# Performance work log

Hardware: AMD Instinct MI355X
Metric: run time of the kernel (lower is better)

## Reference

```python
import jax, jax.numpy as jnp
import numpy as np

KH, KW = 3, 3
STRIDE, PAD, DIL = 1, 1, 1
GROUPS, DG = 1, 1
B, C, H, W = 4, 64, 96, 96
O = 64
K = KH * KW


def setup_inputs() -> dict:
    key = jax.random.key(0)
    k1, k2, k3, k4 = jax.random.split(key, 4)
    x = jax.random.normal(k1, (B, C, H, W), dtype=jnp.float32)
    offset = jax.random.normal(k2, (B, DG * 2 * K, H, W), dtype=jnp.float32)
    mask = jax.random.uniform(k3, (B, DG * K, H, W), dtype=jnp.float32)
    stdv = 1.0 / np.sqrt(C * KH * KW)
    weight = jax.random.uniform(k4, (O, C // GROUPS, KH, KW), dtype=jnp.float32,
                                minval=-stdv, maxval=stdv)
    bias = jnp.zeros((O,), dtype=jnp.float32)
    return {"x": x, "offset": offset, "mask": mask, "weight": weight, "bias": bias}


def _dcn(x, offset, mask, weight, bias):
    Bc, Cc, Hc, Wc = x.shape
    Ho = (Hc + 2 * PAD - DIL * (KH - 1) - 1) // STRIDE + 1
    Wo = (Wc + 2 * PAD - DIL * (KW - 1) - 1) // STRIDE + 1
    Cg = Cc // DG
    dt = x.dtype

    # offset channels per deform group: [k, (y,x)] interleaved (mmcv layout)
    off = offset.reshape(Bc, DG, K, 2, Ho, Wo)
    off_y, off_x = off[:, :, :, 0], off[:, :, :, 1]          # [B,DG,K,Ho,Wo]
    m = mask.reshape(Bc, DG, K, Ho, Wo)

    ky = (jnp.arange(K) // KW).astype(dt) * DIL               # kernel tap dy
    kx = (jnp.arange(K) % KW).astype(dt) * DIL                # kernel tap dx
    base_y = (jnp.arange(Ho) * STRIDE - PAD).astype(dt)
    base_x = (jnp.arange(Wo) * STRIDE - PAD).astype(dt)
    py = base_y[None, None, None, :, None] + ky[None, None, :, None, None] + off_y
    px = base_x[None, None, None, None, :] + kx[None, None, :, None, None] + off_x

    y0 = jnp.floor(py)
    x0 = jnp.floor(px)
    ly = py - y0
    lx = px - x0
    y0i = y0.astype(jnp.int32)
    x0i = x0.astype(jnp.int32)

    x_flat = x.reshape(Bc, DG, Cg, Hc * Wc)

    def gather(yi, xi):
        # zero-padding semantics: out-of-range corners contribute 0
        valid = ((yi >= 0) & (yi < Hc) & (xi >= 0) & (xi < Wc)).astype(dt)
        idx = jnp.clip(yi, 0, Hc - 1) * Wc + jnp.clip(xi, 0, Wc - 1)
        idx_b = jnp.broadcast_to(idx.reshape(Bc, DG, 1, K * Ho * Wo),
                                 (Bc, DG, Cg, K * Ho * Wo))
        vals = jnp.take_along_axis(x_flat, idx_b, axis=3)
        return vals.reshape(Bc, DG, Cg, K, Ho, Wo), valid

    v00, m00 = gather(y0i, x0i)
    v01, m01 = gather(y0i, x0i + 1)
    v10, m10 = gather(y0i + 1, x0i)
    v11, m11 = gather(y0i + 1, x0i + 1)

    w00 = ((1 - ly) * (1 - lx) * m00)[:, :, None]             # [B,DG,1,K,Ho,Wo]
    w01 = ((1 - ly) * lx * m01)[:, :, None]
    w10 = (ly * (1 - lx) * m10)[:, :, None]
    w11 = (ly * lx * m11)[:, :, None]

    sampled = v00 * w00 + v01 * w01 + v10 * w10 + v11 * w11   # bilinear
    sampled = sampled * m[:, :, None]                         # mask modulation
    s = sampled.reshape(Bc, Cc, K, Ho, Wo)

    out = jnp.einsum('ock,bckhw->bohw', weight.reshape(O, Cc, K), s)
    return out + bias[None, :, None, None]


def reference(x, offset, mask, weight, bias):
    return _dcn(x, offset, mask, weight, bias)
```

## Files before the change

kernel.cpp:

```cpp
#include <hip/hip_runtime.h>

#define Bn 4
#define Cn 64
#define Hn 96
#define Wn 96
#define On 64
#define Kn 9
#define HWn (Hn*Wn)
#define NT 256
#define TP 16
#define TW (Wn/TP)
#define TG 3
#define NGRP (TW/TG)
#define NBLK (Bn*Hn*NGRP)
#define WR 9
#define WC 24
#define XSTR 72
#define NPIX (WR*WC)
#define SSTRIDE 584
#define NKT 18

typedef __attribute__((ext_vector_type(8))) short bf16x8;
typedef __attribute__((ext_vector_type(4))) short bf16x4;
typedef __attribute__((ext_vector_type(4))) float f32x4;
typedef __attribute__((ext_vector_type(4))) unsigned u32x4;

__device__ __forceinline__ unsigned short f2bf(float f) {
    unsigned u = __float_as_uint(f);
    u += 0x7FFFu + ((u >> 16) & 1u);
    return (unsigned short)(u >> 16);
}
__device__ __forceinline__ float bf2f(unsigned short h) {
    return __uint_as_float((unsigned)h << 16);
}
__device__ __forceinline__ unsigned cvtpk(float a, float b) {
    return (unsigned)f2bf(a) | ((unsigned)f2bf(b) << 16);
}

__global__ __launch_bounds__(NT, 3) void dcn_fused_kernel(
    const float* __restrict__ x, const float* __restrict__ offset,
    const float* __restrict__ mask, const float* __restrict__ w,
    const float* __restrict__ bias, float* __restrict__ out)
{
    __shared__ __align__(16) unsigned short xwin[NPIX * XSTR];
    __shared__ __align__(16) unsigned short Slds[TP * SSTRIDE];
    __shared__ float4 lwv[4][36];
    __shared__ int    lbs[4][36];

    const int tid  = threadIdx.x;
    const int wave = tid >> 6;
    const int lane = tid & 63;

    const int p = blockIdx.x;
    const int v = (p & 7) * (NBLK / 8) + (p >> 3);
    const int b   = v / (Hn * NGRP);
    int rem       = v - b * (Hn * NGRP);
    const int ho  = rem / NGRP;
    const int grp = rem - ho * NGRP;
    const int wr0 = ho - 4;

    bf16x8 afrag[NKT];
    {
        const float* wrow = w + ((wave * 16 + (lane & 15)) * (Cn * Kn))
                              + ((lane >> 4) * 8);
        #pragma unroll
        for (int t = 0; t < NKT; ++t) {
            float4 fa = *(const float4*)(wrow + t * 32);
            float4 fb = *(const float4*)(wrow + t * 32 + 4);
            u32x4 u;
            u.x = cvtpk(fa.x, fa.y);
            u.y = cvtpk(fa.z, fa.w);
            u.z = cvtpk(fb.x, fb.y);
            u.w = cvtpk(fb.z, fb.w);
            afrag[t] = __builtin_bit_cast(bf16x8, u);
        }
    }

    for (int s = 0; s < TG; ++s) {
        const int wt  = grp * TG + s;
        const int wo0 = wt * TP;
        const int wc0 = wo0 - 4;

        {
            const float* xb = x + (size_t)b * Cn * HWn;
            #pragma unroll 4
            for (int i = 0; i < (Cn / 2 * NPIX) / NT; ++i) {
                int e   = i * NT + tid;
                int cp  = e / NPIX;
                int pix = e - cp * NPIX;
                int r   = pix / WC;
                int col = pix - r * WC;
                int gr = wr0 + r, gc = wc0 + col;
                bool ok = (gr >= 0) && (gr < Hn) && (gc >= 0) && (gc < Wn);
                int cgr = min(max(gr, 0), Hn - 1);
                int cgc = min(max(gc, 0), Wn - 1);
                const float* src = xb + (size_t)(2 * cp) * HWn + cgr * Wn + cgc;
                float v0 = src[0];
                float v1 = src[HWn];
                if (!ok) { v0 = 0.f; v1 = 0.f; }
                *(unsigned*)&xwin[pix * XSTR + 2 * cp] = cvtpk(v0, v1);
            }
        }

        if (lane < 36) {
            const int k  = lane >> 2;
            const int pl = lane & 3;
            const int wo = wo0 + wave * 4 + pl;
            float oy = offset[((b * (2*Kn) + 2*k    ) * Hn + ho) * Wn + wo];
            float ox = offset[((b * (2*Kn) + 2*k + 1) * Hn + ho) * Wn + wo];
            float mm = mask  [((b * Kn + k) * Hn + ho) * Wn + wo];
            float py = (float)(ho - 1 + (k / 3)) + oy;
            float px = (float)(wo - 1 + (k % 3)) + ox;
            float y0f = floorf(py), x0f = floorf(px);
            float ly = py - y0f, lx = px - x0f;
            int y0 = (int)y0f, x0i = (int)x0f;
            float vy0 = (y0     >= 0 && y0     < Hn) ? 1.f : 0.f;
            float vy1 = (y0 + 1 >= 0 && y0 + 1 < Hn) ? 1.f : 0.f;
            float vx0 = (x0i    >= 0 && x0i    < Wn) ? 1.f : 0.f;
            float vx1 = (x0i+ 1 >= 0 && x0i+ 1 < Wn) ? 1.f : 0.f;
            float4 wv;
            wv.x = (1.f - ly) * (1.f - lx) * mm * vy0 * vx0;
            wv.y = (1.f - ly) * lx         * mm * vy0 * vx1;
            wv.z = ly         * (1.f - lx) * mm * vy1 * vx0;
            wv.w = ly         * lx         * mm * vy1 * vx1;
            lwv[wave][lane] = wv;
            int ry = y0 - wr0, rx = x0i - wc0;
            bool fast = (ry >= 0) && (ry <= WR - 2) && (rx >= 0) && (rx <= WC - 2);
            lbs[wave][lane] = fast ? (ry * WC + rx) : -1;
        }
        __syncthreads();

        {
            const int pl  = lane >> 4;
            const int q   = lane & 15;
            const int gpx = wave * 4 + pl;
            unsigned short* Srow = &Slds[gpx * SSTRIDE];
            #pragma unroll
            for (int k = 0; k < Kn; ++k) {
                float4 wv = lwv[wave][k * 4 + pl];
                int base  = lbs[wave][k * 4 + pl];
                float f[4];
                if (base >= 0) {
                    const unsigned short* ppix = &xwin[base * XSTR + q * 4];
                    bf16x4 v0 = *(const bf16x4*)(ppix);
                    bf16x4 v1 = *(const bf16x4*)(ppix + XSTR);
                    bf16x4 v2 = *(const bf16x4*)(ppix + WC * XSTR);
                    bf16x4 v3 = *(const bf16x4*)(ppix + WC * XSTR + XSTR);
                    #pragma unroll
                    for (int j = 0; j < 4; ++j) {
                        f[j] = wv.x * bf2f((unsigned short)v0[j])
                             + wv.y * bf2f((unsigned short)v1[j])
                             + wv.z * bf2f((unsigned short)v2[j])
                             + wv.w * bf2f((unsigned short)v3[j]);
                    }
                } else {
                    const int wo = wo0 + gpx;
                    float oy = offset[((b * (2*Kn) + 2*k    ) * Hn + ho) * Wn + wo];
                    float ox = offset[((b * (2*Kn) + 2*k + 1) * Hn + ho) * Wn + wo];
                    float py = (float)(ho - 1 + (k / 3)) + oy;
                    float px = (float)(wo - 1 + (k % 3)) + ox;
                    int y0 = (int)floorf(py), x0i = (int)floorf(px);
                    int cy0 = min(max(y0,     0), Hn - 1);
                    int cy1 = min(max(y0 + 1, 0), Hn - 1);
                    int cx0 = min(max(x0i,     0), Wn - 1);
                    int cx1 = min(max(x0i + 1, 0), Wn - 1);
                    int i00 = cy0 * Wn + cx0, i01 = cy0 * Wn + cx1;
                    int i10 = cy1 * Wn + cx0, i11 = cy1 * Wn + cx1;
                    const float* xc = x + ((size_t)b * Cn + q * 4) * HWn;
                    #pragma unroll
                    for (int j = 0; j < 4; ++j) {
                        const float* xj = xc + (size_t)j * HWn;
                        f[j] = wv.x * xj[i00] + wv.y * xj[i01]
                             + wv.z * xj[i10] + wv.w * xj[i11];
                    }
                }
                unsigned p01 = cvtpk(f[0], f[1]);
                unsigned p23 = cvtpk(f[2], f[3]);
                Srow[(q * 4 + 0) * Kn + k] = (unsigned short)(p01);
                Srow[(q * 4 + 1) * Kn + k] = (unsigned short)(p01 >> 16);
                Srow[(q * 4 + 2) * Kn + k] = (unsigned short)(p23);
                Srow[(q * 4 + 3) * Kn + k] = (unsigned short)(p23 >> 16);
            }
        }
        __syncthreads();

        {
            const int n    = lane & 15;
            const int quad = lane >> 4;
            f32x4 acc = {0.f, 0.f, 0.f, 0.f};
            #pragma unroll
            for (int t = 0; t < NKT; ++t) {
                bf16x8 bFrag = *(const bf16x8*)&Slds[n * SSTRIDE + t * 32 + quad * 8];
                acc = __builtin_amdgcn_mfma_f32_16x16x32_bf16(afrag[t], bFrag, acc, 0, 0, 0);
            }
            #pragma unroll
            for (int r = 0; r < 4; ++r) {
                int o = wave * 16 + quad * 4 + r;
                out[(((size_t)b * On + o) * Hn + ho) * Wn + wo0 + n] = acc[r] + bias[o];
            }
        }
    }
}

extern "C" void kernel_launch(void* const* d_in, const int* in_sizes, int n_in,
                              void* d_out, int out_size, void* d_ws, size_t ws_size,
                              hipStream_t stream) {
    (void)in_sizes; (void)n_in; (void)out_size; (void)d_ws; (void)ws_size;
    dcn_fused_kernel<<<NBLK, NT, 0, stream>>>(
        (const float*)d_in[0], (const float*)d_in[1], (const float*)d_in[2],
        (const float*)d_in[3], (const float*)d_in[4], (float*)d_out);
}
```

Baseline: 109.5 us.

## Reorder GEMM reduction to tap-major, vectorize S stores, restructure window load

Result: no change. 107.7 us (-1.6%).

```diff
diff --git a/kernel.cpp b/kernel.cpp
--- a/kernel.cpp
+++ b/kernel.cpp
@@ -15,7 +15,7 @@
 #define NBLK (Bn*Hn*NGRP)
 #define WR 9
 #define WC 24
-#define XSTR 72
+#define XSTR 68
 #define NPIX (WR*WC)
 #define SSTRIDE 584
 #define NKT 18
@@ -61,17 +61,20 @@
 
     bf16x8 afrag[NKT];
     {
-        const float* wrow = w + ((wave * 16 + (lane & 15)) * (Cn * Kn))
-                              + ((lane >> 4) * 8);
+        const int o  = wave * 16 + (lane & 15);
+        const int hi = lane >> 4;
+        const float* wlane = w + (size_t)o * (Cn * Kn) + hi * 8 * Kn;
         #pragma unroll
         for (int t = 0; t < NKT; ++t) {
-            float4 fa = *(const float4*)(wrow + t * 32);
-            float4 fb = *(const float4*)(wrow + t * 32 + 4);
+            const float* src = wlane + (t & 1) * 32 * Kn + (t >> 1);
+            float f[8];
+            #pragma unroll
+            for (int j = 0; j < 8; ++j) f[j] = src[j * Kn];
             u32x4 u;
-            u.x = cvtpk(fa.x, fa.y);
-            u.y = cvtpk(fa.z, fa.w);
-            u.z = cvtpk(fb.x, fb.y);
-            u.w = cvtpk(fb.z, fb.w);
+            u.x = cvtpk(f[0], f[1]);
+            u.y = cvtpk(f[2], f[3]);
+            u.z = cvtpk(f[4], f[5]);
+            u.w = cvtpk(f[6], f[7]);
             afrag[t] = __builtin_bit_cast(bf16x8, u);
         }
     }
@@ -81,24 +84,23 @@
         const int wo0 = wt * TP;
         const int wc0 = wo0 - 4;
 
-        {
-            const float* xb = x + (size_t)b * Cn * HWn;
-            #pragma unroll 4
-            for (int i = 0; i < (Cn / 2 * NPIX) / NT; ++i) {
-                int e   = i * NT + tid;
-                int cp  = e / NPIX;
-                int pix = e - cp * NPIX;
-                int r   = pix / WC;
-                int col = pix - r * WC;
-                int gr = wr0 + r, gc = wc0 + col;
-                bool ok = (gr >= 0) && (gr < Hn) && (gc >= 0) && (gc < Wn);
-                int cgr = min(max(gr, 0), Hn - 1);
-                int cgc = min(max(gc, 0), Wn - 1);
-                const float* src = xb + (size_t)(2 * cp) * HWn + cgr * Wn + cgc;
-                float v0 = src[0];
-                float v1 = src[HWn];
-                if (!ok) { v0 = 0.f; v1 = 0.f; }
-                *(unsigned*)&xwin[pix * XSTR + 2 * cp] = cvtpk(v0, v1);
+        if (tid < NPIX) {
+            const int r   = tid / WC;
+            const int col = tid - r * WC;
+            const int gr = wr0 + r, gc = wc0 + col;
+            unsigned short* dst = &xwin[tid * XSTR];
+            if ((gr >= 0) & (gr < Hn) & (gc >= 0) & (gc < Wn)) {
+                const float* src = x + (size_t)b * Cn * HWn + gr * Wn + gc;
+                #pragma unroll 8
+                for (int cp = 0; cp < Cn / 2; ++cp) {
+                    float v0 = src[(2 * cp) * HWn];
+                    float v1 = src[(2 * cp + 1) * HWn];
+                    *(unsigned*)&dst[2 * cp] = cvtpk(v0, v1);
+                }
+            } else {
+                #pragma unroll 8
+                for (int cp = 0; cp < Cn / 2; ++cp)
+                    *(unsigned*)&dst[2 * cp] = 0u;
             }
         }
 
@@ -174,12 +176,10 @@
                              + wv.z * xj[i10] + wv.w * xj[i11];
                     }
                 }
-                unsigned p01 = cvtpk(f[0], f[1]);
-                unsigned p23 = cvtpk(f[2], f[3]);
-                Srow[(q * 4 + 0) * Kn + k] = (unsigned short)(p01);
-                Srow[(q * 4 + 1) * Kn + k] = (unsigned short)(p01 >> 16);
-                Srow[(q * 4 + 2) * Kn + k] = (unsigned short)(p23);
-                Srow[(q * 4 + 3) * Kn + k] = (unsigned short)(p23 >> 16);
+                uint2 pk;
+                pk.x = cvtpk(f[0], f[1]);
+                pk.y = cvtpk(f[2], f[3]);
+                *(uint2*)&Slds[gpx * SSTRIDE + k * 64 + q * 4] = pk;
             }
         }
         __syncthreads();
```
